# Optimization experiments

Hardware: AMD Instinct MI355X
Metric: run time of the kernel (lower is better)

The kernel has to match this reference:

```python
import jax, jax.numpy as jnp
import numpy as np

DIM = 1024; HEADS = 8; DHEAD = 64; INNER = HEADS * DHEAD
WS = 512; B = 2; N = 2048; FF = 4 * DIM
NEG = -1e9


def layernorm(x, g, b, eps=1e-5):
    mu = jnp.mean(x, -1, keepdims=True)
    var = jnp.mean((x - mu) ** 2, -1, keepdims=True)
    return (x - mu) * jax.lax.rsqrt(var + eps) * g + b


def rmsnorm(x, g, eps=1e-6):
    return x * jax.lax.rsqrt(jnp.mean(x * x, -1, keepdims=True) + eps) * g


def rotate_half(x):
    x1, x2 = jnp.split(x, 2, -1)
    return jnp.concatenate([-x2, x1], -1)


def local_attention(q, k, v):
    # lucidrains LocalAttention: single-head over last dim, rotary pos emb,
    # window_size=WS, causal, look_backward=1, look_forward=0. n % WS == 0 so autopad no-op.
    b, n, d = q.shape
    w = n // WS
    inv_freq = 1.0 / (10000.0 ** (jnp.arange(0, d, 2, dtype=jnp.float32) / d))
    t = jnp.arange(n)
    freqs = t[:, None].astype(jnp.float32) * inv_freq[None, :]
    emb = jnp.concatenate([freqs, freqs], -1)           # [n, d]
    cos, sin = jnp.cos(emb), jnp.sin(emb)
    q = q * cos + rotate_half(q) * sin
    k = k * cos + rotate_half(k) * sin
    bq = q.reshape(b, w, WS, d) * (d ** -0.5)
    bk = k.reshape(b, w, WS, d)
    bv = v.reshape(b, w, WS, d)

    def look_around(x, pad_value):
        # gather current window + 1 window backward along the window axis
        pads = [(0, 0), (1, 0)] + [(0, 0)] * (x.ndim - 2)
        xp = jnp.pad(x, pads, constant_values=pad_value)
        return jnp.concatenate([xp[:, 0:w], xp[:, 1:w + 1]], axis=2)

    bk = look_around(bk, 0.0)                 # [b, w, 2*WS, d]
    bv = look_around(bv, 0.0)
    bt = t.reshape(w, WS)                     # query positions per window
    bqk = look_around(bt[None], -1)[0]        # key positions, pad = -1  [w, 2*WS]
    sim = jnp.einsum('bwie,bwje->bwij', bq, bk)  # [b, w, WS, 2*WS]
    mask = (bt[:, :, None] < bqk[:, None, :]) | (bqk[:, None, :] == -1)
    sim = jnp.where(mask[None], NEG, sim)
    attn = jax.nn.softmax(sim, -1)
    out = jnp.einsum('bwij,bwje->bwie', attn, bv)
    return out.reshape(b, n, d)


def setup_inputs() -> dict:
    key = jax.random.key(0)
    ks = jax.random.split(key, 10)
    s = 0.02
    f32 = jnp.float32
    return {
        'text': jax.random.normal(ks[0], (B, N, DIM), f32),
        'audio': jax.random.normal(ks[1], (B, N, DIM), f32),
        'video': jax.random.normal(ks[2], (B, N, DIM), f32),
        'Wa': jax.random.normal(ks[3], (DIM, DIM), f32) * s,
        'ba': jnp.zeros((DIM,), f32),
        'lna_g': jnp.ones((DIM,), f32), 'lna_b': jnp.zeros((DIM,), f32),
        'Wvid': jax.random.normal(ks[4], (DIM, DIM), f32) * s,
        'bvid': jnp.zeros((DIM,), f32),
        'lnv_g': jnp.ones((DIM,), f32), 'lnv_b': jnp.zeros((DIM,), f32),
        'ln1_g': jnp.ones((DIM,), f32), 'ln1_b': jnp.zeros((DIM,), f32),
        'Wq': jax.random.normal(ks[5], (DIM, INNER), f32) * s,
        'Wkv': jax.random.normal(ks[6], (DIM, 2 * INNER), f32) * s,
        'qn_g': jnp.ones((DHEAD,), f32), 'kn_g': jnp.ones((DHEAD,), f32),
        'Wo': jax.random.normal(ks[7], (INNER, DIM), f32) * s,
        'W1': jax.random.normal(ks[8], (DIM, FF), f32) * s,
        'b1': jnp.zeros((FF,), f32),
        'ln2_g': jnp.ones((FF,), f32), 'ln2_b': jnp.zeros((FF,), f32),
        'W2': jax.random.normal(ks[9], (FF, DIM), f32) * s,
        'b2': jnp.zeros((DIM,), f32),
    }


def reference(text, audio, video, Wa, ba, lna_g, lna_b, Wvid, bvid, lnv_g, lnv_b,
              ln1_g, ln1_b, Wq, Wkv, qn_g, kn_g, Wo, W1, b1, ln2_g, ln2_b, W2, b2):
    # modality -> text-token adapters (audio_to_text / video_to_text): linear + layernorm
    audio_t = layernorm(audio @ Wa + ba, lna_g, lna_b)
    video_t = layernorm(video @ Wvid + bvid, lnv_g, lnv_b)
    # windowed local attention: q=text, k=audio tokens, v=video tokens
    x = local_attention(text, audio_t, video_t)          # [B, N, DIM]
    # qk-norm full causal attention (flash=False: dense [B,H,N,N] scores)
    b, n, _ = x.shape
    h = layernorm(x, ln1_g, ln1_b)
    q = (h @ Wq).reshape(b, n, HEADS, DHEAD).transpose(0, 2, 1, 3)
    k, v = jnp.split(h @ Wkv, 2, -1)
    k = k.reshape(b, n, HEADS, DHEAD).transpose(0, 2, 1, 3)
    v = v.reshape(b, n, HEADS, DHEAD).transpose(0, 2, 1, 3)
    q = rmsnorm(q, qn_g)
    k = rmsnorm(k, kn_g)
    sim = jnp.einsum('bhid,bhjd->bhij', q, k) * (DHEAD ** -0.5)
    causal = jnp.tril(jnp.ones((n, n), bool))
    sim = jnp.where(causal[None, None], sim, NEG)
    attn = jax.nn.softmax(sim, -1)
    o = jnp.einsum('bhij,bhjd->bhid', attn, v).transpose(0, 2, 1, 3).reshape(b, n, INNER)
    x = o @ Wo
    x = x + x                                            # x = x + x in source
    # FFN: Linear -> GELU -> post-act LayerNorm -> Linear, + residual
    h1 = layernorm(jax.nn.gelu(x @ W1 + b1), ln2_g, ln2_b)
    return h1 @ W2 + b2 + x
```

## Files before the change

### kernel.cpp

```cpp
#include <hip/hip_runtime.h>
#include <hip/hip_bf16.h>

typedef __bf16 bf16;
typedef __bf16 bf16x8 __attribute__((ext_vector_type(8)));
typedef float  f32x4  __attribute__((ext_vector_type(4)));

static __device__ __forceinline__ float b2f(bf16 x) { return (float)x; }
static __device__ __forceinline__ bf16  f2b(float x) { return (bf16)x; }
static __device__ __forceinline__ float ldval(float v) { return v; }
static __device__ __forceinline__ float ldval(bf16 v)  { return (float)v; }

static __device__ __forceinline__ void gl_lds16(const bf16* g, bf16* l)
{
    __builtin_amdgcn_global_load_lds(
        (const __attribute__((address_space(1))) void*)g,
        (__attribute__((address_space(3))) void*)l,
        16, 0, 0);
}

__global__ void detect_dtype(const unsigned short* __restrict__ p, int* __restrict__ flag)
{
    if (threadIdx.x == 0 && blockIdx.x == 0) {
        int big = 0;
        for (int i = 0; i < 512; ++i) {
            int e = (p[i] >> 7) & 0xFF;
            if (e >= 0xE0) big++;
        }
        *flag = (big > 0) ? 1 : 0;
    }
}

__global__ __launch_bounds__(256) void convert2(
    const void* __restrict__ sa, const void* __restrict__ sb,
    bf16* __restrict__ da, bf16* __restrict__ db, int n,
    const int* __restrict__ flag)
{
    int f = *flag;
    int half = gridDim.x >> 1;
    const void* s = (blockIdx.x < half) ? sa : sb;
    bf16* d = (blockIdx.x < half) ? da : db;
    int bid = (blockIdx.x < half) ? blockIdx.x : blockIdx.x - half;
    for (int i = bid * 256 + threadIdx.x; i < n; i += half * 256) {
        float v = f ? ((const float*)s)[i] : (float)((const bf16*)s)[i];
        d[i] = f2b(v);
    }
}

struct VecPack { const void* src[14]; int n[14]; };
__global__ __launch_bounds__(256) void convert_vecs(
    VecPack vp, bf16* __restrict__ dst, const int* __restrict__ flag)
{
    int v = blockIdx.x;
    int f = *flag;
    const void* s = vp.src[v];
    int n = vp.n[v];
    bf16* d = dst + (size_t)v * 4096;
    for (int i = threadIdx.x; i < n; i += 256) {
        float x = f ? ((const float*)s)[i] : (float)((const bf16*)s)[i];
        d[i] = f2b(x);
    }
}

template <int EPI, int MT>
__global__ __launch_bounds__(256) void gemm_bt(
    const bf16* __restrict__ A0, int lda, int zsA, int zsA2,
    const bf16* __restrict__ B0, int ldb, int zsB, int zsB2,
    void* __restrict__ C0, int ldc, int zsC, int zsC2,
    const bf16* __restrict__ bias, int zsBias, float scale, int K)
{
    constexpr int IFR = MT / 32;
    __shared__ __align__(16) bf16 As[MT * 64];
    __shared__ __align__(16) bf16 Bs[128 * 64];
    const int z = blockIdx.z;
    const bf16* A  = A0 + (size_t)z * zsA + (size_t)(z >> 2) * zsA2;
    const bf16* Bt = B0 + (size_t)z * zsB + (size_t)(z >> 2) * zsB2;
    const size_t cbase = (size_t)z * zsC + (size_t)(z >> 2) * zsC2;
    if (bias) bias += (size_t)z * zsBias;
    const int tid  = threadIdx.x;
    const int lane = tid & 63, wave = tid >> 6;
    const int quad = lane >> 4, l16 = lane & 15;
    const size_t tm = (size_t)blockIdx.y * MT, tn = (size_t)blockIdx.x * 128;
    const int wm = (wave >> 1) * (MT / 2), wn = (wave & 1) * 64;
    const int srow = lane >> 3;
    const int scol = ((lane & 7) ^ srow) * 8;

    f32x4 acc[IFR][4];
    const f32x4 zro = {0.f, 0.f, 0.f, 0.f};
    #pragma unroll
    for (int i = 0; i < IFR; ++i)
        #pragma unroll
        for (int j = 0; j < 4; ++j) acc[i][j] = zro;

    const int swzA = l16 & 7;
    for (int k0 = 0; k0 < K; k0 += 64) {
        #pragma unroll
        for (int i = 0; i < IFR; ++i) {
            int chunk = (wave * IFR + i) * 64;
            int row = (chunk >> 3) + srow;
            gl_lds16(A + (tm + row) * (size_t)lda + k0 + scol, As + (size_t)chunk * 8);
        }
        #pragma unroll
        for (int i = 0; i < 4; ++i) {
            int chunk = (wave * 4 + i) * 64;
            int row = (chunk >> 3) + srow;
            gl_lds16(Bt + (tn + row) * (size_t)ldb + k0 + scol, Bs + (size_t)chunk * 8);
        }
        __syncthreads();
        #pragma unroll
        for (int kk = 0; kk < 2; ++kk) {
            bf16x8 af[IFR], bfr[4];
            #pragma unroll
            for (int i = 0; i < IFR; ++i) {
                int row = wm + i * 16 + l16;
                af[i] = *(const bf16x8*)(const void*)&As[(row * 8 + ((kk*4 + quad) ^ swzA)) * 8];
            }
            #pragma unroll
            for (int j = 0; j < 4; ++j) {
                int row = wn + j * 16 + l16;
                bfr[j] = *(const bf16x8*)(const void*)&Bs[(row * 8 + ((kk*4 + quad) ^ swzA)) * 8];
            }
            #pragma unroll
            for (int i = 0; i < IFR; ++i)
                #pragma unroll
                for (int j = 0; j < 4; ++j)
                    acc[i][j] = __builtin_amdgcn_mfma_f32_16x16x32_bf16(
                        af[i], bfr[j], acc[i][j], 0, 0, 0);
        }
        __syncthreads();
    }

    float* Cf = (float*)C0;
    bf16*  Cb = (bf16*)C0;
    #pragma unroll
    for (int i = 0; i < IFR; ++i) {
        #pragma unroll
        for (int j = 0; j < 4; ++j) {
            size_t col = tn + wn + j*16 + l16;
            float bb = bias ? b2f(bias[col]) : 0.f;
            #pragma unroll
            for (int r = 0; r < 4; ++r) {
                size_t row = tm + wm + i*16 + quad*4 + r;
                float v = acc[i][j][r] + bb;
                size_t off = cbase + row * (size_t)ldc + col;
                if (EPI == 0) {
                    Cf[off] = v;
                } else if (EPI == 1) {
                    Cb[off] = f2b(v * scale);
                } else {
                    float g = 0.5f * v * (1.f + tanhf(0.7978845608028654f *
                                  (v + 0.044715f * v * v * v)));
                    Cb[off] = f2b(g);
                }
            }
        }
    }
}

__global__ void transpose_any(const void* __restrict__ in, int R, int C,
                              unsigned short* __restrict__ out, int ldo,
                              const int* __restrict__ flag)
{
    __shared__ unsigned short t[32][33];
    int f = *flag;
    int c0 = blockIdx.x * 32, r0 = blockIdx.y * 32;
    int tx = threadIdx.x, ty = threadIdx.y;
    for (int i = ty; i < 32; i += 8) {
        size_t idx = (size_t)(r0 + i) * C + c0 + tx;
        bf16 v = f ? f2b(((const float*)in)[idx]) : ((const bf16*)in)[idx];
        t[i][tx] = *(unsigned short*)&v;
    }
    __syncthreads();
    for (int i = ty; i < 32; i += 8)
        out[(size_t)(c0 + i) * ldo + r0 + tx] = t[tx][i];
}

__global__ void transpose_vt(const unsigned short* __restrict__ in,
                             unsigned short* __restrict__ out)
{
    __shared__ unsigned short t[32][33];
    int b = blockIdx.z;
    const unsigned short* src = in + (size_t)b * 2048 * 1024;
    unsigned short* dst = out + (size_t)b * 1024 * 2560;
    int c0 = blockIdx.x * 32, r0 = blockIdx.y * 32;
    int tx = threadIdx.x, ty = threadIdx.y;
    for (int i = ty; i < 32; i += 8)
        t[i][tx] = src[(size_t)(r0 + i) * 1024 + c0 + tx];
    __syncthreads();
    for (int i = ty; i < 32; i += 8)
        dst[(size_t)(c0 + i) * 2560 + 512 + r0 + tx] = t[tx][i];
}

__global__ void transpose_v(const float* __restrict__ qkv, bf16* __restrict__ Vt)
{
    __shared__ float t[32][33];
    int bh = blockIdx.z, b = bh >> 3, h = bh & 7;
    const float* src = qkv + (size_t)b * 2048 * 1536 + 1024 + h * 64;
    int c0 = blockIdx.x * 32, r0 = blockIdx.y * 32;
    int tx = threadIdx.x, ty = threadIdx.y;
    for (int i = ty; i < 32; i += 8)
        t[i][tx] = src[(size_t)(r0 + i) * 1536 + c0 + tx];
    __syncthreads();
    bf16* dst = Vt + (size_t)bh * 64 * 2048;
    for (int i = ty; i < 32; i += 8)
        dst[(size_t)(c0 + i) * 2048 + r0 + tx] = f2b(t[tx][i]);
}

template <typename Tin>
__global__ __launch_bounds__(256) void ln_rows(
    const Tin* __restrict__ in, int C,
    const bf16* __restrict__ g, const bf16* __restrict__ b,
    bf16* __restrict__ out, float eps)
{
    const int row = blockIdx.x, tid = threadIdx.x;
    const Tin* p = in + (size_t)row * C;
    float s = 0.f, ss = 0.f;
    for (int c = tid; c < C; c += 256) {
        float v = ldval(p[c]);
        s += v; ss += v * v;
    }
    #pragma unroll
    for (int d = 32; d > 0; d >>= 1) { s += __shfl_xor(s, d); ss += __shfl_xor(ss, d); }
    __shared__ float red[2][4];
    int wave = tid >> 6, lane = tid & 63;
    if (lane == 0) { red[0][wave] = s; red[1][wave] = ss; }
    __syncthreads();
    s  = red[0][0] + red[0][1] + red[0][2] + red[0][3];
    ss = red[1][0] + red[1][1] + red[1][2] + red[1][3];
    float mu   = s / C;
    float var  = ss / C - mu * mu;
    float rstd = rsqrtf(var + eps);
    bf16* q = out + (size_t)row * C;
    for (int c = tid; c < C; c += 256) {
        float v = ldval(p[c]);
        q[c] = f2b((v - mu) * rstd * b2f(g[c]) + b2f(b[c]));
    }
}

__global__ __launch_bounds__(256) void ln_rows2(
    const bf16* __restrict__ in,
    const bf16* __restrict__ g0, const bf16* __restrict__ b0,
    const bf16* __restrict__ g1, const bf16* __restrict__ b1,
    bf16* __restrict__ out0, bf16* __restrict__ out1)
{
    const int row = blockIdx.x, tid = threadIdx.x;
    const int sel = row >> 12;
    const bf16* p = in + (size_t)row * 1024;
    const bf16* g = sel ? g1 : g0;
    const bf16* b = sel ? b1 : b0;
    bf16* q = (sel ? out1 + (size_t)(row - 4096) * 1024 : out0 + (size_t)row * 1024);
    float s = 0.f, ss = 0.f;
    for (int c = tid; c < 1024; c += 256) {
        float v = b2f(p[c]);
        s += v; ss += v * v;
    }
    #pragma unroll
    for (int d = 32; d > 0; d >>= 1) { s += __shfl_xor(s, d); ss += __shfl_xor(ss, d); }
    __shared__ float red[2][4];
    int wave = tid >> 6, lane = tid & 63;
    if (lane == 0) { red[0][wave] = s; red[1][wave] = ss; }
    __syncthreads();
    s  = red[0][0] + red[0][1] + red[0][2] + red[0][3];
    ss = red[1][0] + red[1][1] + red[1][2] + red[1][3];
    float mu   = s * (1.f / 1024.f);
    float var  = ss * (1.f / 1024.f) - mu * mu;
    float rstd = rsqrtf(var + 1e-5f);
    for (int c = tid; c < 1024; c += 256) {
        float v = b2f(p[c]);
        q[c] = f2b((v - mu) * rstd * b2f(g[c]) + b2f(b[c]));
    }
}

__global__ __launch_bounds__(256) void rotary_kernel(
    const void* __restrict__ text, const int* __restrict__ flag,
    const bf16* __restrict__ audioT,
    bf16* __restrict__ qrot, bf16* __restrict__ krotPad)
{
    int row = blockIdx.x;
    int t = row & 2047, b = row >> 11;
    int tid = threadIdx.x;
    int f = *flag;
    const float lg = 9.210340371976184f / 512.f;
    size_t base = (size_t)row * 1024;
    size_t kb = ((size_t)(b * 2560 + 512 + t)) * 1024;
    for (int c = tid; c < 512; c += 256) {
        float invf = __expf(-(float)c * lg);
        float th = (float)t * invf;
        float sn, cs;
        sincosf(th, &sn, &cs);
        float q1 = f ? ((const float*)text)[base + c]
                     : b2f(((const bf16*)text)[base + c]);
        float q2 = f ? ((const float*)text)[base + c + 512]
                     : b2f(((const bf16*)text)[base + c + 512]);
        qrot[base + c]       = f2b((q1 * cs - q2 * sn) * 0.03125f);
        qrot[base + c + 512] = f2b((q2 * cs + q1 * sn) * 0.03125f);
        float k1 = b2f(audioT[base + c]), k2 = b2f(audioT[base + c + 512]);
        krotPad[kb + c]       = f2b(k1 * cs - k2 * sn);
        krotPad[kb + c + 512] = f2b(k2 * cs + k1 * sn);
    }
}

__global__ __launch_bounds__(256) void softmax_local(
    const float* __restrict__ sim, bf16* __restrict__ attn)
{
    int i  = blockIdx.x;
    int zz = blockIdx.y;
    int w  = zz & 3;
    int tid = threadIdx.x;
    const float* p = sim + ((size_t)zz * 512 + i) * 1024;
    bf16* q = attn + ((size_t)zz * 512 + i) * 1024;
    int jlo = (w == 0) ? 512 : 0;
    int jhi = 512 + i;
    float m = -1e30f;
    #pragma unroll
    for (int k = 0; k < 4; ++k) {
        int c = tid + k * 256;
        if (c >= jlo && c <= jhi) m = fmaxf(m, p[c]);
    }
    #pragma unroll
    for (int d = 32; d > 0; d >>= 1) m = fmaxf(m, __shfl_xor(m, d));
    __shared__ float red[2][4];
    int wave = tid >> 6, lane = tid & 63;
    if (lane == 0) red[0][wave] = m;
    __syncthreads();
    m = fmaxf(fmaxf(red[0][0], red[0][1]), fmaxf(red[0][2], red[0][3]));
    float pv[4];
    float s = 0.f;
    #pragma unroll
    for (int k = 0; k < 4; ++k) {
        int c = tid + k * 256;
        float e = (c >= jlo && c <= jhi) ? __expf(p[c] - m) : 0.f;
        pv[k] = e; s += e;
    }
    #pragma unroll
    for (int d = 32; d > 0; d >>= 1) s += __shfl_xor(s, d);
    if (lane == 0) red[1][wave] = s;
    __syncthreads();
    s = red[1][0] + red[1][1] + red[1][2] + red[1][3];
    float inv = 1.f / s;
    #pragma unroll
    for (int k = 0; k < 4; ++k) q[tid + k * 256] = f2b(pv[k] * inv);
}

__global__ __launch_bounds__(256) void pack_qk(
    const float* __restrict__ qkv, bf16* __restrict__ Qp, bf16* __restrict__ Kp,
    const bf16* __restrict__ qn_g, const bf16* __restrict__ kn_g)
{
    int gid  = blockIdx.x * 4 + (threadIdx.x >> 6);
    int lane = threadIdx.x & 63;
    int token = gid >> 4, r = gid & 15, part = r >> 3, h = r & 7;
    const float* p = qkv + (size_t)token * 1536 + part * 512 + h * 64 + lane;
    float v = *p;
    float ss = v * v;
    #pragma unroll
    for (int d = 32; d > 0; d >>= 1) ss += __shfl_xor(ss, d);
    float sc = rsqrtf(ss * (1.f / 64.f) + 1e-6f);
    const bf16* gw = part ? kn_g : qn_g;
    float outv = v * sc * b2f(gw[lane]);
    if (!part) outv *= 0.125f;
    int b = token >> 11, t = token & 2047;
    bf16* dst = (part ? Kp : Qp) + ((size_t)(b * 8 + h) * 2048 + t) * 64 + lane;
    *dst = f2b(outv);
}

__global__ __launch_bounds__(256) void flash_split(
    const bf16* __restrict__ Qp, const bf16* __restrict__ Kp,
    const bf16* __restrict__ Vt, bf16* __restrict__ o,
    float* __restrict__ Opart, float* __restrict__ MLpart)
{
    const int qb = blockIdx.x;
    const int chunk = blockIdx.y;
    const int nch = (qb >> 3) + 1;
    if (chunk >= nch) return;
    __shared__ __align__(16) bf16 Ks[64][72];
    __shared__ __align__(16) bf16 Vs[64][72];
    __shared__ __align__(16) bf16 Ps[4][16][72];
    const int bh = blockIdx.z, b = bh >> 3, h = bh & 7;
    const int qm = qb * 64;
    const int jt0 = chunk * 512;
    const int jt1 = min(jt0 + 512, qm + 64);
    const int tid = threadIdx.x, wave = tid >> 6, lane = tid & 63;
    const int quad = lane >> 4, l16 = lane & 15;
    const bf16* Qg = Qp + (size_t)bh * 2048 * 64;
    const bf16* Kg = Kp + (size_t)bh * 2048 * 64;
    const bf16* Vg = Vt + (size_t)bh * 64 * 2048;

    const int qrow = qm + wave * 16 + l16;
    bf16x8 qa[2];
    qa[0] = *(const bf16x8*)(const void*)(Qg + (size_t)qrow * 64 + quad * 8);
    qa[1] = *(const bf16x8*)(const void*)(Qg + (size_t)qrow * 64 + 32 + quad * 8);

    f32x4 oacc[4];
    const f32x4 zro = {0.f, 0.f, 0.f, 0.f};
    #pragma unroll
    for (int j = 0; j < 4; ++j) oacc[j] = zro;
    float mst[4] = {-1e30f, -1e30f, -1e30f, -1e30f};
    float lst[4] = {0.f, 0.f, 0.f, 0.f};

    const int ldr = tid >> 2, ldc = (tid & 3) * 16;
    for (int jt = jt0; jt < jt1; jt += 64) {
        *(uint4*)(void*)&Ks[ldr][ldc] =
            *(const uint4*)(const void*)(Kg + (size_t)(jt + ldr) * 64 + ldc);
        *(uint4*)(void*)&Ks[ldr][ldc + 8] =
            *(const uint4*)(const void*)(Kg + (size_t)(jt + ldr) * 64 + ldc + 8);
        *(uint4*)(void*)&Vs[ldr][ldc] =
            *(const uint4*)(const void*)(Vg + (size_t)ldr * 2048 + jt + ldc);
        *(uint4*)(void*)&Vs[ldr][ldc + 8] =
            *(const uint4*)(const void*)(Vg + (size_t)ldr * 2048 + jt + ldc + 8);
        __syncthreads();

        f32x4 s[4];
        #pragma unroll
        for (int j = 0; j < 4; ++j) s[j] = zro;
        #pragma unroll
        for (int kk = 0; kk < 2; ++kk) {
            #pragma unroll
            for (int j = 0; j < 4; ++j) {
                bf16x8 kb = *(const bf16x8*)(const void*)&Ks[j*16 + l16][kk*32 + quad*8];
                s[j] = __builtin_amdgcn_mfma_f32_16x16x32_bf16(qa[kk], kb, s[j], 0, 0, 0);
            }
        }

        if (jt + 63 > qm + wave * 16) {
            #pragma unroll
            for (int j = 0; j < 4; ++j) {
                int key = jt + j * 16 + l16;
                #pragma unroll
                for (int r = 0; r < 4; ++r) {
                    int row = qm + wave * 16 + quad * 4 + r;
                    if (key > row) s[j][r] = -1e30f;
                }
            }
        }

        f32x4 tmax = s[0];
        #pragma unroll
        for (int j = 1; j < 4; ++j)
            #pragma unroll
            for (int r = 0; r < 4; ++r) tmax[r] = fmaxf(tmax[r], s[j][r]);
        #pragma unroll
        for (int r = 0; r < 4; ++r) {
            float tv = tmax[r];
            #pragma unroll
            for (int d = 1; d < 16; d <<= 1) tv = fmaxf(tv, __shfl_xor(tv, d));
            tmax[r] = tv;
        }
        float scl[4];
        #pragma unroll
        for (int r = 0; r < 4; ++r) {
            float mn = fmaxf(mst[r], tmax[r]);
            scl[r] = __expf(mst[r] - mn);
            mst[r] = mn;
        }
        f32x4 psum = zro;
        #pragma unroll
        for (int j = 0; j < 4; ++j)
            #pragma unroll
            for (int r = 0; r < 4; ++r) {
                float e = __expf(s[j][r] - mst[r]);
                s[j][r] = e;
                psum[r] += e;
            }
        #pragma unroll
        for (int r = 0; r < 4; ++r) {
            float tv = psum[r];
            #pragma unroll
            for (int d = 1; d < 16; d <<= 1) tv += __shfl_xor(tv, d);
            lst[r] = lst[r] * scl[r] + tv;
        }
        #pragma unroll
        for (int j = 0; j < 4; ++j)
            #pragma unroll
            for (int r = 0; r < 4; ++r) oacc[j][r] *= scl[r];

        #pragma unroll
        for (int j = 0; j < 4; ++j)
            #pragma unroll
            for (int r = 0; r < 4; ++r)
                Ps[wave][quad*4 + r][j*16 + l16] = f2b(s[j][r]);
        bf16x8 pa[2];
        pa[0] = *(const bf16x8*)(const void*)&Ps[wave][l16][quad*8];
        pa[1] = *(const bf16x8*)(const void*)&Ps[wave][l16][32 + quad*8];

        #pragma unroll
        for (int kk = 0; kk < 2; ++kk) {
            #pragma unroll
            for (int j = 0; j < 4; ++j) {
                bf16x8 vb = *(const bf16x8*)(const void*)&Vs[j*16 + l16][kk*32 + quad*8];
                oacc[j] = __builtin_amdgcn_mfma_f32_16x16x32_bf16(pa[kk], vb, oacc[j], 0, 0, 0);
            }
        }
        __syncthreads();
    }

    if (nch == 1) {
        #pragma unroll
        for (int j = 0; j < 4; ++j) {
            #pragma unroll
            for (int r = 0; r < 4; ++r) {
                int t = qm + wave * 16 + quad * 4 + r;
                o[((size_t)(b * 2048 + t)) * 512 + h * 64 + j * 16 + l16] =
                    f2b(oacc[j][r] / lst[r]);
            }
        }
    } else {
        int pidx = (bh * 32 + qb) * 4 + chunk;
        float* Od = Opart + (size_t)pidx * 4096;
        #pragma unroll
        for (int j = 0; j < 4; ++j)
            #pragma unroll
            for (int r = 0; r < 4; ++r) {
                int row = wave * 16 + quad * 4 + r;
                Od[row * 64 + j * 16 + l16] = oacc[j][r];
            }
        if (l16 == 0) {
            #pragma unroll
            for (int r = 0; r < 4; ++r) {
                int row = wave * 16 + quad * 4 + r;
                MLpart[(size_t)pidx * 128 + row]      = mst[r];
                MLpart[(size_t)pidx * 128 + 64 + row] = lst[r];
            }
        }
    }
}

__global__ __launch_bounds__(256) void flash_combine(
    const float* __restrict__ Opart, const float* __restrict__ MLpart,
    bf16* __restrict__ o)
{
    int qb = blockIdx.x + 8;
    int bh = blockIdx.y, b = bh >> 3, h = bh & 7;
    int nch = (qb >> 3) + 1;
    int row = threadIdx.x >> 2;
    int d0 = (threadIdx.x & 3) * 16;
    int base = (bh * 32 + qb) * 4;
    float m[4], l[4], w[4];
    float mstar = -1e30f;
    for (int c = 0; c < nch; ++c) {
        m[c] = MLpart[(size_t)(base + c) * 128 + row];
        l[c] = MLpart[(size_t)(base + c) * 128 + 64 + row];
        mstar = fmaxf(mstar, m[c]);
    }
    float lstar = 0.f;
    for (int c = 0; c < nch; ++c) {
        w[c] = __expf(m[c] - mstar);
        lstar += l[c] * w[c];
    }
    float inv = 1.f / lstar;
    int t = qb * 64 + row;
    bf16* op = o + ((size_t)(b * 2048 + t)) * 512 + h * 64 + d0;
    #pragma unroll 4
    for (int dd = 0; dd < 16; ++dd) {
        float acc = 0.f;
        for (int c = 0; c < nch; ++c)
            acc += Opart[(size_t)(base + c) * 4096 + row * 64 + d0 + dd] * w[c];
        op[dd] = f2b(acc * inv);
    }
}

__global__ __launch_bounds__(256) void combine_ff2(
    const float* __restrict__ p0, const float* __restrict__ p1,
    const bf16* __restrict__ x2, const bf16* __restrict__ b2,
    float* __restrict__ out)
{
    int i4 = (blockIdx.x * 256 + threadIdx.x) * 4;
    #pragma unroll
    for (int k = 0; k < 4; ++k) {
        int i = i4 + k;
        out[i] = p0[i] + p1[i] + b2f(x2[i]) + b2f(b2[i & 1023]);
    }
}

static void launch_gemm(int epi, hipStream_t s,
                        const bf16* A, int lda, int zsA, int zsA2,
                        const bf16* Bt, int ldb, int zsB, int zsB2,
                        void* C, int ldc, int zsC, int zsC2,
                        const bf16* bias, int zsBias, float scale,
                        int M, int N, int K, int nz)
{
    bool mt64 = ((M >> 7) * (N >> 7) * nz) <= 512;
    dim3 blk(256);
    if (mt64) {
        dim3 g(N / 128, M / 64, nz);
        switch (epi) {
        case 0: gemm_bt<0,64><<<g, blk, 0, s>>>(A, lda, zsA, zsA2, Bt, ldb, zsB, zsB2, C, ldc, zsC, zsC2, bias, zsBias, scale, K); break;
        case 1: gemm_bt<1,64><<<g, blk, 0, s>>>(A, lda, zsA, zsA2, Bt, ldb, zsB, zsB2, C, ldc, zsC, zsC2, bias, zsBias, scale, K); break;
        default: gemm_bt<2,64><<<g, blk, 0, s>>>(A, lda, zsA, zsA2, Bt, ldb, zsB, zsB2, C, ldc, zsC, zsC2, bias, zsBias, scale, K); break;
        }
    } else {
        dim3 g(N / 128, M / 128, nz);
        switch (epi) {
        case 0: gemm_bt<0,128><<<g, blk, 0, s>>>(A, lda, zsA, zsA2, Bt, ldb, zsB, zsB2, C, ldc, zsC, zsC2, bias, zsBias, scale, K); break;
        case 1: gemm_bt<1,128><<<g, blk, 0, s>>>(A, lda, zsA, zsA2, Bt, ldb, zsB, zsB2, C, ldc, zsC, zsC2, bias, zsBias, scale, K); break;
        default: gemm_bt<2,128><<<g, blk, 0, s>>>(A, lda, zsA, zsA2, Bt, ldb, zsB, zsB2, C, ldc, zsC, zsC2, bias, zsBias, scale, K); break;
        }
    }
}

extern "C" void kernel_launch(void* const* d_in, const int* in_sizes, int n_in,
                              void* d_out, int out_size, void* d_ws, size_t ws_size,
                              hipStream_t stream)
{
    const void* text  = d_in[0];
    const void* audio = d_in[1];
    const void* video = d_in[2];
    const void* Wa    = d_in[3];
    const void* ba    = d_in[4];
    const void* lna_g = d_in[5];
    const void* lna_b = d_in[6];
    const void* Wvid  = d_in[7];
    const void* bvid  = d_in[8];
    const void* lnv_g = d_in[9];
    const void* lnv_b = d_in[10];
    const void* ln1_g = d_in[11];
    const void* ln1_b = d_in[12];
    const void* Wq    = d_in[13];
    const void* Wkv   = d_in[14];
    const void* qn_g  = d_in[15];
    const void* kn_g  = d_in[16];
    const void* Wo    = d_in[17];
    const void* W1    = d_in[18];
    const void* b1    = d_in[19];
    const void* ln2_g = d_in[20];
    const void* ln2_b = d_in[21];
    const void* W2    = d_in[22];
    const void* b2    = d_in[23];

    char* ws = (char*)d_ws;
    size_t off = 0;
    auto alloc = [&](size_t bytes) -> char* {
        char* p = ws + off;
        off += (bytes + 255) & ~(size_t)255;
        return p;
    };
    const size_t MB = 1024 * 1024;
    int*  flag  = (int*)alloc(256);
    bf16* vecs  = (bf16*)alloc(14 * 4096 * 2);
    bf16* WqkvT = (bf16*)alloc((size_t)1536 * 1024 * 2);
    bf16* WoT   = (bf16*)alloc((size_t)1024 * 512 * 2);
    bf16* W1T   = (bf16*)alloc((size_t)4096 * 1024 * 2);
    bf16* W2T   = (bf16*)alloc((size_t)1024 * 4096 * 2);
    char* regionIn = alloc(24 * MB);
    char* region2  = alloc(32 * MB);
    char* regionH  = alloc(8 * MB);
    char* regionX  = alloc(8 * MB);
    char* regionO  = alloc(4 * MB);
    bf16* qrot    = (bf16*)alloc((size_t)4096 * 1024 * 2);
    bf16* krotPad = (bf16*)alloc((size_t)2 * 2560 * 1024 * 2);
    bf16* VTpad   = (bf16*)alloc((size_t)2 * 1024 * 2560 * 2);
    bf16* attn    = (bf16*)alloc((size_t)8 * 512 * 1024 * 2);

    bf16*  audioC = (bf16*)regionIn;
    bf16*  videoC = audioC + (size_t)4096 * 1024;
    float* qkvF   = (float*)regionIn;
    bf16*  tmp2   = (bf16*)region2;
    float* tmpF   = (float*)region2;
    float* xF     = (float*)(region2 + 16 * MB);
    bf16*  g      = (bf16*)region2;
    bf16*  audioT = (bf16*)regionH;
    bf16*  h      = (bf16*)regionH;
    bf16*  videoT = (bf16*)regionX;
    bf16*  x2     = (bf16*)regionX;
    bf16*  WaT    = (bf16*)regionO;
    bf16*  WvT    = WaT + (size_t)1024 * 1024;
    bf16*  o      = (bf16*)regionO;
    bf16*  Qp     = qrot;
    bf16*  Kp     = krotPad;
    bf16*  Vth    = attn;
    float* Opart  = (float*)regionIn;
    float* MLpart = Opart + (size_t)16 * 32 * 4 * 4096;
    float* p0     = (float*)regionIn;
    float* p1     = (float*)VTpad;

    bf16* baC   = vecs + 0 * 4096;
    bf16* bvidC = vecs + 1 * 4096;
    bf16* lnagC = vecs + 2 * 4096;
    bf16* lnabC = vecs + 3 * 4096;
    bf16* lnvgC = vecs + 4 * 4096;
    bf16* lnvbC = vecs + 5 * 4096;
    bf16* ln1gC = vecs + 6 * 4096;
    bf16* ln1bC = vecs + 7 * 4096;
    bf16* qngC  = vecs + 8 * 4096;
    bf16* kngC  = vecs + 9 * 4096;
    bf16* b1C   = vecs + 10 * 4096;
    bf16* ln2gC = vecs + 11 * 4096;
    bf16* ln2bC = vecs + 12 * 4096;
    bf16* b2C   = vecs + 13 * 4096;

    detect_dtype<<<1, 64, 0, stream>>>((const unsigned short*)text, flag);

    const int NTOK = 4096 * 1024;
    convert2<<<4096, 256, 0, stream>>>(audio, video, audioC, videoC, NTOK, flag);
    VecPack vp;
    const void* vsrc[14] = {ba, bvid, lna_g, lna_b, lnv_g, lnv_b, ln1_g, ln1_b,
                            qn_g, kn_g, b1, ln2_g, ln2_b, b2};
    int vn[14] = {1024, 1024, 1024, 1024, 1024, 1024, 1024, 1024,
                  64, 64, 4096, 4096, 4096, 1024};
    for (int i = 0; i < 14; ++i) { vp.src[i] = vsrc[i]; vp.n[i] = vn[i]; }
    convert_vecs<<<14, 256, 0, stream>>>(vp, vecs, flag);

    dim3 tb(32, 8);
    transpose_any<<<dim3(32, 32), tb, 0, stream>>>(Wa, 1024, 1024, (unsigned short*)WaT, 1024, flag);
    transpose_any<<<dim3(32, 32), tb, 0, stream>>>(Wvid, 1024, 1024, (unsigned short*)WvT, 1024, flag);
    transpose_any<<<dim3(16, 32), tb, 0, stream>>>(Wq, 1024, 512, (unsigned short*)WqkvT, 1024, flag);
    transpose_any<<<dim3(32, 32), tb, 0, stream>>>(Wkv, 1024, 1024, (unsigned short*)(WqkvT + (size_t)512 * 1024), 1024, flag);
    transpose_any<<<dim3(32, 16), tb, 0, stream>>>(Wo, 512, 1024, (unsigned short*)WoT, 512, flag);
    transpose_any<<<dim3(128, 32), tb, 0, stream>>>(W1, 1024, 4096, (unsigned short*)W1T, 1024, flag);
    transpose_any<<<dim3(32, 128), tb, 0, stream>>>(W2, 4096, 1024, (unsigned short*)W2T, 4096, flag);

    launch_gemm(1, stream, audioC, 1024, 4096*1024, 0, WaT, 1024, 1024*1024, 0,
                tmp2, 1024, 4096*1024, 0, baC, 4096, 1.f, 4096, 1024, 1024, 2);
    ln_rows2<<<8192, 256, 0, stream>>>(tmp2, lnagC, lnabC, lnvgC, lnvbC, audioT, videoT);

    hipMemsetAsync(krotPad, 0, (size_t)2 * 2560 * 1024 * 2, stream);
    hipMemsetAsync(VTpad, 0, (size_t)2 * 1024 * 2560 * 2, stream);
    rotary_kernel<<<4096, 256, 0, stream>>>(text, flag, audioT, qrot, krotPad);
    transpose_vt<<<dim3(32, 64, 2), tb, 0, stream>>>(
        (const unsigned short*)videoT, (unsigned short*)VTpad);

    launch_gemm(0, stream, qrot, 1024, 512*1024, 0,
                krotPad, 1024, 512*1024, 512*1024,
                tmpF, 1024, 512*1024, 0, nullptr, 0, 1.f, 512, 1024, 1024, 8);
    softmax_local<<<dim3(512, 8), 256, 0, stream>>>(tmpF, attn);
    launch_gemm(0, stream, attn, 1024, 512*1024, 0,
                VTpad, 2560, 512, 1024*2560 - 2048,
                xF, 1024, 512*1024, 0, nullptr, 0, 1.f, 512, 1024, 1024, 8);

    ln_rows<float><<<4096, 256, 0, stream>>>(xF, 1024, ln1gC, ln1bC, h, 1e-5f);
    launch_gemm(0, stream, h, 1024, 0, 0, WqkvT, 1024, 0, 0,
                qkvF, 1536, 0, 0, nullptr, 0, 1.f, 4096, 1536, 1024, 1);
    pack_qk<<<16384, 256, 0, stream>>>(qkvF, Qp, Kp, qngC, kngC);
    transpose_v<<<dim3(2, 64, 16), tb, 0, stream>>>(qkvF, Vth);
    flash_split<<<dim3(32, 4, 16), 256, 0, stream>>>(Qp, Kp, Vth, o, Opart, MLpart);
    flash_combine<<<dim3(24, 16), 256, 0, stream>>>(Opart, MLpart, o);

    launch_gemm(1, stream, o, 512, 0, 0, WoT, 512, 0, 0,
                x2, 1024, 0, 0, nullptr, 0, 2.f, 4096, 1024, 512, 1);
    launch_gemm(2, stream, x2, 1024, 0, 0, W1T, 1024, 0, 0,
                g, 4096, 0, 0, b1C, 0, 1.f, 4096, 4096, 1024, 1);
    ln_rows<bf16><<<4096, 256, 0, stream>>>(g, 4096, ln2gC, ln2bC, g, 1e-5f);
    launch_gemm(0, stream, g, 4096, 2048, 0, W2T, 4096, 2048, 0,
                p0, 1024, (int)(p1 - p0), 0, nullptr, 0, 1.f, 4096, 1024, 2048, 2);
    combine_ff2<<<4096, 256, 0, stream>>>(p0, p1, x2, b2C, (float*)d_out);

    (void)in_sizes; (void)n_in; (void)out_size; (void)ws_size;
}
```

Baseline: 603.8 us.

## Add dedicated 256x256 eight-wave GEMM for FF1 with fused GELU epilogue

Replaces the generic GEMM for the FFN first projection (4096x4096x1024) with a specialized kernel that uses 256x256 tiles, 8 waves, double-buffered LDS filled by direct global-to-LDS loads with an XOR swizzle, and prefetch interleaved across four MFMA phases with priority raising. The GELU epilogue switches from tanhf to an equivalent sigmoid form built on __expf. The larger tiles raise data reuse, but the grid shrinks to 256 blocks and each thread carries 32 accumulator vectors, which strains registers and occupancy.

```diff
diff --git a/kernel.cpp b/kernel.cpp
--- a/kernel.cpp
+++ b/kernel.cpp
@@ -151,6 +151,120 @@
                                   (v + 0.044715f * v * v * v)));
                     Cb[off] = f2b(g);
                 }
+            }
+        }
+    }
+}
+
+__global__ __launch_bounds__(512, 2) void gemm_ff1_8ph(
+    const bf16* __restrict__ A, int lda,
+    const bf16* __restrict__ Bt, int ldb,
+    bf16* __restrict__ C, int ldc,
+    const bf16* __restrict__ bias, int K)
+{
+    __shared__ __align__(16) bf16 As[2][256 * 64];
+    __shared__ __align__(16) bf16 Bs[2][256 * 64];
+    const int tid  = threadIdx.x;
+    const int lane = tid & 63, wave = tid >> 6;
+    const int quad = lane >> 4, l16 = lane & 15;
+    const int wr = wave >> 2, wc = wave & 3;
+    const size_t tm = (size_t)blockIdx.y * 256;
+    const size_t tn = (size_t)blockIdx.x * 256;
+    const int srow = lane >> 3;
+    const int scol = ((lane & 7) ^ srow) * 8;
+    const int swz  = l16 & 7;
+
+    f32x4 acc[8][4];
+    const f32x4 zro = {0.f, 0.f, 0.f, 0.f};
+    #pragma unroll
+    for (int m = 0; m < 8; ++m)
+        #pragma unroll
+        for (int n = 0; n < 4; ++n) acc[m][n] = zro;
+
+    const bf16* aSrc[4];
+    const bf16* bSrc[4];
+    #pragma unroll
+    for (int i = 0; i < 4; ++i) {
+        int grow = wave * 32 + i * 8 + srow;
+        aSrc[i] = A  + (tm + grow) * (size_t)lda + scol;
+        bSrc[i] = Bt + (tn + grow) * (size_t)ldb + scol;
+    }
+
+#define STAGE(BUF, K0, I)                                                     \
+    do {                                                                      \
+        gl_lds16(aSrc[I] + (K0), &As[BUF][(wave * 4 + (I)) * 512]);           \
+        gl_lds16(bSrc[I] + (K0), &Bs[BUF][(wave * 4 + (I)) * 512]);           \
+    } while (0)
+
+#define LDA_F(BUF, M, KK)                                                     \
+    (*(const bf16x8*)(const void*)&As[BUF][(wr * 128 + (M) * 16 + l16) * 64 + \
+        ((((KK) * 4 + quad) ^ swz) << 3)])
+#define LDB_F(BUF, N, KK)                                                     \
+    (*(const bf16x8*)(const void*)&Bs[BUF][(wc * 64 + (N) * 16 + l16) * 64 +  \
+        ((((KK) * 4 + quad) ^ swz) << 3)])
+
+#define PHASE(M0, M1, PREF_STMT, TAIL_STMT)                                   \
+    {                                                                         \
+        PREF_STMT;                                                            \
+        bf16x8 x0 = LDA_F(cur, M0, 0), x1 = LDA_F(cur, M0, 1);                \
+        bf16x8 y0 = LDA_F(cur, M1, 0), y1 = LDA_F(cur, M1, 1);                \
+        asm volatile("s_barrier" ::: "memory");                               \
+        __builtin_amdgcn_s_setprio(1);                                        \
+        _Pragma("unroll")                                                     \
+        for (int n = 0; n < 4; ++n) {                                         \
+            acc[M0][n] = __builtin_amdgcn_mfma_f32_16x16x32_bf16(x0, bfr[n][0], acc[M0][n], 0, 0, 0); \
+            acc[M0][n] = __builtin_amdgcn_mfma_f32_16x16x32_bf16(x1, bfr[n][1], acc[M0][n], 0, 0, 0); \
+            acc[M1][n] = __builtin_amdgcn_mfma_f32_16x16x32_bf16(y0, bfr[n][0], acc[M1][n], 0, 0, 0); \
+            acc[M1][n] = __builtin_amdgcn_mfma_f32_16x16x32_bf16(y1, bfr[n][1], acc[M1][n], 0, 0, 0); \
+        }                                                                     \
+        __builtin_amdgcn_s_setprio(0);                                        \
+        TAIL_STMT;                                                            \
+        asm volatile("s_barrier" ::: "memory");                               \
+    }
+
+    #pragma unroll
+    for (int i = 0; i < 4; ++i) STAGE(0, 0, i);
+    asm volatile("s_waitcnt vmcnt(0)" ::: "memory");
+    asm volatile("s_barrier" ::: "memory");
+
+    const int NT = K >> 6;
+    bf16x8 bfr[4][2];
+    for (int t = 0; t < NT; ++t) {
+        const int cur = t & 1, nxt = cur ^ 1;
+        const int k1  = (t + 1) << 6;
+        const bool pref = (t + 1 < NT);
+
+        #pragma unroll
+        for (int n = 0; n < 4; ++n) {
+            bfr[n][0] = LDB_F(cur, n, 0);
+            bfr[n][1] = LDB_F(cur, n, 1);
+        }
+        PHASE(0, 1,
+              if (pref) { STAGE(nxt, k1, 0); STAGE(nxt, k1, 1); }, )
+        PHASE(2, 3,
+              if (pref) { STAGE(nxt, k1, 2); STAGE(nxt, k1, 3); }, )
+        PHASE(4, 5, , )
+        PHASE(6, 7, ,
+              asm volatile("s_waitcnt vmcnt(0)" ::: "memory"))
+    }
+#undef PHASE
+#undef LDB_F
+#undef LDA_F
+#undef STAGE
+
+    #pragma unroll
+    for (int m = 0; m < 8; ++m) {
+        #pragma unroll
+        for (int n = 0; n < 4; ++n) {
+            size_t col = tn + wc * 64 + n * 16 + l16;
+            float bb = b2f(bias[col]);
+            #pragma unroll
+            for (int r = 0; r < 4; ++r) {
+                size_t row = tm + wr * 128 + m * 16 + quad * 4 + r;
+                float v = acc[m][n][r] + bb;
+                float s = v * (1.5957691216057308f + 0.07135481627f * v * v);
+                float g = v / (1.f + __expf(-s));
+                C[row * (size_t)ldc + col] = f2b(g);
             }
         }
     }
@@ -735,8 +849,8 @@
 
     launch_gemm(1, stream, o, 512, 0, 0, WoT, 512, 0, 0,
                 x2, 1024, 0, 0, nullptr, 0, 2.f, 4096, 1024, 512, 1);
-    launch_gemm(2, stream, x2, 1024, 0, 0, W1T, 1024, 0, 0,
-                g, 4096, 0, 0, b1C, 0, 1.f, 4096, 4096, 1024, 1);
+    gemm_ff1_8ph<<<dim3(16, 16), 512, 0, stream>>>(x2, 1024, W1T, 1024,
+                                                   g, 4096, b1C, 1024);
     ln_rows<bf16><<<4096, 256, 0, stream>>>(g, 4096, ln2gC, ln2bC, g, 1e-5f);
     launch_gemm(0, stream, g, 4096, 2048, 0, W2T, 4096, 2048, 0,
                 p0, 1024, (int)(p1 - p0), 0, nullptr, 0, 1.f, 4096, 1024, 2048, 2);
```

New measurement: 612.7 us. Within noise of the previous version (+1.5%).
